# Performance work log

Hardware: AMD Instinct MI355X
Metric: run time of the kernel (lower is better)

Reference implementation:

```python
import jax, jax.numpy as jnp
import numpy as np

B, T, IN, H, L = 256, 80, 39, 256, 5


def _xavier(key, shape):
    fan_out, fan_in = shape[0], shape[1]
    std = (2.0 / (fan_in + fan_out)) ** 0.5
    return std * jax.random.normal(key, shape, dtype=jnp.float32)


def setup_inputs() -> dict:
    key = jax.random.key(0)
    ks = jax.random.split(key, 4 + 2 * L)
    x = jax.random.normal(ks[0], (B, T, IN), dtype=jnp.float32)
    # PyTorch LSTM params, gate order (i, f, g, o); biases zero per init.
    W_ih0 = _xavier(ks[1], (4 * H, IN))                       # layer 0 input weights
    W_ih_rest = jnp.stack([_xavier(ks[2 + l], (4 * H, H)) for l in range(L - 1)])  # [L-1,4H,H]
    W_hh = jnp.stack([_xavier(ks[1 + L + l], (4 * H, H)) for l in range(L)])       # [L,4H,H]
    b_ih = jnp.zeros((L, 4 * H), dtype=jnp.float32)
    b_hh = jnp.zeros((L, 4 * H), dtype=jnp.float32)
    fc_w = _xavier(ks[2 * L + 1], (1, H))
    fc_b = jnp.zeros((1,), dtype=jnp.float32)
    return {"x": x, "W_ih0": W_ih0, "W_ih_rest": W_ih_rest, "W_hh": W_hh,
            "b_ih": b_ih, "b_hh": b_hh, "fc_w": fc_w, "fc_b": fc_b}


def _lstm_layer(xs, W_ih, W_hh_l, b_ih_l, b_hh_l):
    # xs: [B,T,D]. Precompute input projection for all timesteps (one big GEMM).
    x_proj = jnp.einsum('btd,gd->btg', xs, W_ih) + b_ih_l + b_hh_l  # [B,T,4H]

    def step(carry, xp):
        h, c = carry
        gates = xp + h @ W_hh_l.T                 # [B,4H]
        i, f, g, o = jnp.split(gates, 4, axis=-1)
        c = jax.nn.sigmoid(f) * c + jax.nn.sigmoid(i) * jnp.tanh(g)
        h = jax.nn.sigmoid(o) * jnp.tanh(c)
        return (h, c), h

    b = xs.shape[0]
    h0 = jnp.zeros((b, H), dtype=xs.dtype)
    _, hs = jax.lax.scan(step, (h0, h0), jnp.swapaxes(x_proj, 0, 1))
    return jnp.swapaxes(hs, 0, 1)  # [B,T,H]


def reference(x, W_ih0, W_ih_rest, W_hh, b_ih, b_hh, fc_w, fc_b):
    h = _lstm_layer(x, W_ih0, W_hh[0], b_ih[0], b_hh[0])
    for l in range(1, L):
        h = _lstm_layer(h, W_ih_rest[l - 1], W_hh[l], b_ih[l], b_hh[l])
    out = jnp.einsum('bth,oh->bto', h, fc_w) + fc_b  # [B,T,1]
    return out[..., 0]  # [B,T]
```

## Files before the change

### kernel.cpp

```cpp
#include <hip/hip_runtime.h>

#define B_ 256
#define T_ 80
#define IN_ 39
#define H_ 256
#define G_ 1024
#define L_ 5
#define TC_ 16
#define NCH_ 5

#define XP_FLOATS   (B_ * TC_ * G_)
#define HBUF_FLOATS (B_ * T_ * H_)
#define CBUF_FLOATS (B_ * H_)
#define WG_FLOATS   (L_ * G_ * H_)
#define HX_FLOATS   (2 * 32 * 2048)
#define FLG_OFF_FLOATS (XP_FLOATS + HBUF_FLOATS + CBUF_FLOATS + WG_FLOATS + HX_FLOATS)

#define AG __HIP_MEMORY_SCOPE_AGENT
#define WG __HIP_MEMORY_SCOPE_WORKGROUP

__device__ __forceinline__ float sigm(float x) { return 1.0f / (1.0f + expf(-x)); }
__device__ __forceinline__ void fma4(float4& a, float s, const float4& w) {
    a.x = fmaf(s, w.x, a.x); a.y = fmaf(s, w.y, a.y);
    a.z = fmaf(s, w.z, a.z); a.w = fmaf(s, w.w, a.w);
}
__device__ __forceinline__ void red4(float4& a) {
    a.x += __shfl_xor(a.x, 32); a.y += __shfl_xor(a.y, 32);
    a.z += __shfl_xor(a.z, 32); a.w += __shfl_xor(a.w, 32);
}

__device__ __forceinline__ float4 ld_mall_16B(const float* p) {
    float4 v;
    asm volatile("global_load_dwordx4 %0, %1, off sc0 sc1\n\t"
                 "s_waitcnt vmcnt(0)"
                 : "=&v"(v) : "v"(p) : "memory");
    return v;
}

__device__ __forceinline__ void cbar(int* cnt, int& seq) {
    seq += 4;
    asm volatile("s_waitcnt lgkmcnt(0)" ::: "memory");
    if ((threadIdx.x & 63) == 0)
        __hip_atomic_fetch_add(cnt, 1, __ATOMIC_RELAXED, WG);
    while (__hip_atomic_load(cnt, __ATOMIC_RELAXED, WG) < seq)
        __builtin_amdgcn_s_sleep(1);
    asm volatile("s_waitcnt lgkmcnt(0)" ::: "memory");
}

extern "C" __global__ void __launch_bounds__(256)
wt_kernel(const float* __restrict__ Whh, float* __restrict__ Wg) {
    const int gid = blockIdx.x * 256 + threadIdx.x;
    const int g4 = gid & 3;
    const int j  = (gid >> 2) & 31;
    const int k  = (gid >> 7) & 255;
    const int s  = (gid >> 15) & 7;
    const int l  = gid >> 18;
    Wg[gid] = Whh[((size_t)(l * 1024 + g4 * 256 + s * 32 + j)) * 256 + k];
}

extern "C" __global__ void __launch_bounds__(256)
proj_kernel(const float* __restrict__ src, const float* __restrict__ Wih,
            const float* __restrict__ bihl, const float* __restrict__ bhhl,
            float* __restrict__ xp, int K, int t0) {
    __shared__ float As[16 * 132];
    __shared__ float Bs[16 * 68];
    const int tid = threadIdx.x;
    const int mt = blockIdx.x >> 4, nt = blockIdx.x & 15;
    const int tx = tid & 15, ty = tid >> 4;
    const int lrA = tid >> 1, lc8 = (tid & 1) * 8;
    const int lrB = tid >> 2, lc4 = (tid & 3) * 4;

    const int ar = mt * 128 + lrA;
    const int ab = ar >> 4;
    const int at = t0 + (ar & 15);
    const float* arow = src + ((size_t)ab * T_ + at) * K;
    const int brow_idx = (lrB & 3) * 256 + nt * 16 + (lrB >> 2);
    const float* brow = Wih + (size_t)brow_idx * K;

    float acc[8][4];
    #pragma unroll
    for (int i = 0; i < 8; ++i)
        #pragma unroll
        for (int j = 0; j < 4; ++j) acc[i][j] = 0.0f;

    for (int k0 = 0; k0 < K; k0 += 16) {
        __syncthreads();
        if (K == IN_) {
            #pragma unroll
            for (int i = 0; i < 8; ++i) {
                const int k = k0 + lc8 + i;
                As[(lc8 + i) * 132 + lrA] = (k < IN_) ? arow[k] : 0.0f;
            }
            #pragma unroll
            for (int i = 0; i < 4; ++i) {
                const int k = k0 + lc4 + i;
                Bs[(lc4 + i) * 68 + lrB] = (k < IN_) ? brow[k] : 0.0f;
            }
        } else {
            float4 a0 = *(const float4*)(arow + k0 + lc8);
            float4 a1 = *(const float4*)(arow + k0 + lc8 + 4);
            As[(lc8 + 0) * 132 + lrA] = a0.x;
            As[(lc8 + 1) * 132 + lrA] = a0.y;
            As[(lc8 + 2) * 132 + lrA] = a0.z;
            As[(lc8 + 3) * 132 + lrA] = a0.w;
            As[(lc8 + 4) * 132 + lrA] = a1.x;
            As[(lc8 + 5) * 132 + lrA] = a1.y;
            As[(lc8 + 6) * 132 + lrA] = a1.z;
            As[(lc8 + 7) * 132 + lrA] = a1.w;
            float4 bv = *(const float4*)(brow + k0 + lc4);
            Bs[(lc4 + 0) * 68 + lrB] = bv.x;
            Bs[(lc4 + 1) * 68 + lrB] = bv.y;
            Bs[(lc4 + 2) * 68 + lrB] = bv.z;
            Bs[(lc4 + 3) * 68 + lrB] = bv.w;
        }
        __syncthreads();
        #pragma unroll
        for (int kk = 0; kk < 16; ++kk) {
            const float4 aA = *(const float4*)&As[kk * 132 + ty * 8];
            const float4 aB = *(const float4*)&As[kk * 132 + ty * 8 + 4];
            const float4 b4 = *(const float4*)&Bs[kk * 68 + tx * 4];
            acc[0][0] += aA.x * b4.x; acc[0][1] += aA.x * b4.y;
            acc[0][2] += aA.x * b4.z; acc[0][3] += aA.x * b4.w;
            acc[1][0] += aA.y * b4.x; acc[1][1] += aA.y * b4.y;
            acc[1][2] += aA.y * b4.z; acc[1][3] += aA.y * b4.w;
            acc[2][0] += aA.z * b4.x; acc[2][1] += aA.z * b4.y;
            acc[2][2] += aA.z * b4.z; acc[2][3] += aA.z * b4.w;
            acc[3][0] += aA.w * b4.x; acc[3][1] += aA.w * b4.y;
            acc[3][2] += aA.w * b4.z; acc[3][3] += aA.w * b4.w;
            acc[4][0] += aB.x * b4.x; acc[4][1] += aB.x * b4.y;
            acc[4][2] += aB.x * b4.z; acc[4][3] += aB.x * b4.w;
            acc[5][0] += aB.y * b4.x; acc[5][1] += aB.y * b4.y;
            acc[5][2] += aB.y * b4.z; acc[5][3] += aB.y * b4.w;
            acc[6][0] += aB.z * b4.x; acc[6][1] += aB.z * b4.y;
            acc[6][2] += aB.z * b4.z; acc[6][3] += aB.z * b4.w;
            acc[7][0] += aB.w * b4.x; acc[7][1] += aB.w * b4.y;
            acc[7][2] += aB.w * b4.z; acc[7][3] += aB.w * b4.w;
        }
    }
    const int unit = nt * 16 + tx;
    const float bs0 = bihl[0 * 256 + unit] + bhhl[0 * 256 + unit];
    const float bs1 = bihl[1 * 256 + unit] + bhhl[1 * 256 + unit];
    const float bs2 = bihl[2 * 256 + unit] + bhhl[2 * 256 + unit];
    const float bs3 = bihl[3 * 256 + unit] + bhhl[3 * 256 + unit];
    #pragma unroll
    for (int i = 0; i < 8; ++i) {
        const int row = mt * 128 + ty * 8 + i;
        float4 o;
        o.x = acc[i][0] + bs0; o.y = acc[i][1] + bs1;
        o.z = acc[i][2] + bs2; o.w = acc[i][3] + bs3;
        *(float4*)&xp[(size_t)row * G_ + unit * 4] = o;
    }
}

extern "C" __global__ void __launch_bounds__(512, 2)
rec10_kernel(const float* __restrict__ xp, const float* __restrict__ Wg_l,
             float* __restrict__ hbuf, float* __restrict__ cbuf,
             float* __restrict__ hx, int* __restrict__ flg,
             int t0, int chkb, int first) {
    __shared__ float sH[2048];
    __shared__ float sP[2 * 4 * 32 * 20];
    __shared__ int   barC[2];

    const int tid = threadIdx.x;
    const int bid = blockIdx.x;
    const int grp = bid & 31;
    const int s   = bid >> 5;
    const int c   = tid >> 8;
    const int tp  = tid & 255;
    const int jj  = tp & 31;
    const int ks  = tp >> 5;
    const int w4  = tp >> 6;
    const int fb2 = tp >> 5;
    const int unit = s * 32 + jj;
    const int bglob = grp * 8 + c * 4 + (fb2 & 3);
    float* sPc = sP + c * 2560;
    int* mycnt = barC + c;
    int* flgc  = flg + (grp * 2 + c) * 32;

    if (tid < 2) barC[tid] = 0;

    const float4* Wg4 = (const float4*)Wg_l + (size_t)s * 8192;
    float4 wreg[32];
    #pragma unroll
    for (int kk = 0; kk < 32; ++kk)
        wreg[kk] = Wg4[(size_t)(ks * 32 + kk) * 32 + jj];

    float creg = 0.0f;
    if (tp < 128 && !first) creg = cbuf[(size_t)bglob * H_ + unit];

    __syncthreads();

    const float4* sH4 = (const float4*)sH;
    int seq = 0;

    for (int tt = 0; tt < TC_; ++tt) {
        const int t = t0 + tt;

        float4 xv = make_float4(0.f, 0.f, 0.f, 0.f);
        if (tp < 128)
            xv = *(const float4*)&xp[((size_t)bglob * TC_ + tt) * G_ + unit * 4];

        if (tt == 0) {
            if (first) {
                *(float4*)&sH[tp * 8 + c * 4] = make_float4(0.f, 0.f, 0.f, 0.f);
            } else {
                #pragma unroll
                for (int bb = 0; bb < 4; ++bb)
                    sH[tp * 8 + c * 4 + bb] =
                        hbuf[((size_t)(grp * 8 + c * 4 + bb) * T_ + (t0 - 1)) * H_ + tp];
            }
        } else {
            if ((tid & 63) < 8) {
                int* fp = flgc + (tid & 63);
                const int tgt = chkb + tt;
                while (__hip_atomic_load(fp, __ATOMIC_RELAXED, AG) < tgt)
                    __builtin_amdgcn_s_sleep(1);
            }
            const float* hsf = hx + (size_t)(((tt - 1) & 1) * 32 + grp) * 2048
                                  + (size_t)tp * 8 + c * 4;
            *(float4*)&sH[tp * 8 + c * 4] = ld_mall_16B(hsf);
        }
        cbar(mycnt, seq);

        float4 a0 = {0,0,0,0}, a1 = {0,0,0,0}, a2 = {0,0,0,0}, a3 = {0,0,0,0};
        #pragma unroll
        for (int kk = 0; kk < 32; ++kk) {
            const int k = ks * 32 + kk;
            const float4 wv = wreg[kk];
            const float4 hc = sH4[k * 2 + c];
            fma4(a0, hc.x, wv); fma4(a1, hc.y, wv);
            fma4(a2, hc.z, wv); fma4(a3, hc.w, wv);
        }
        red4(a0); red4(a1); red4(a2); red4(a3);
        if ((tid & 63) < 32) {
            float4* pp = (float4*)&sPc[(w4 * 32 + jj) * 20];
            pp[0] = a0; pp[1] = a1; pp[2] = a2; pp[3] = a3;
        }
        cbar(mycnt, seq);

        if (tp < 128) {
            float4 g4 = xv;
            #pragma unroll
            for (int w2 = 0; w2 < 4; ++w2) {
                const float4 pw = *(const float4*)&sPc[(w2 * 32 + jj) * 20 + fb2 * 4];
                g4.x += pw.x; g4.y += pw.y; g4.z += pw.z; g4.w += pw.w;
            }
            const float I = sigm(g4.x);
            const float F = sigm(g4.y);
            const float Gt = tanhf(g4.z);
            const float O = sigm(g4.w);
            creg = F * creg + I * Gt;
            const float hval = O * tanhf(creg);
            hbuf[((size_t)bglob * T_ + t) * H_ + unit] = hval;

            if (tt < TC_ - 1) {
                const float hpart = __shfl_xor(hval, 32);
                if ((fb2 & 1) == 0) {
                    const unsigned long long pv =
                        ((unsigned long long)__float_as_uint(hpart) << 32)
                        | __float_as_uint(hval);
                    unsigned long long* dst = (unsigned long long*)
                        (hx + (size_t)((tt & 1) * 32 + grp) * 2048
                            + unit * 8 + c * 4 + fb2);
                    __hip_atomic_store(dst, pv, __ATOMIC_RELAXED, AG);
                }
            }
        }

        if (tt < TC_ - 1) {
            asm volatile("s_waitcnt vmcnt(0)" ::: "memory");
            cbar(mycnt, seq);
            if (tp == 0)
                __hip_atomic_store(flgc + s, chkb + tt + 1, __ATOMIC_RELAXED, AG);
        }
    }

    if (tp < 128) cbuf[(size_t)bglob * H_ + unit] = creg;
}

extern "C" __global__ void __launch_bounds__(128)
fc_kernel(const float* __restrict__ hbuf, const float* __restrict__ fcw,
          const float* __restrict__ fcb, float* __restrict__ out) {
    __shared__ float wsm[256];
    const int tid = threadIdx.x;
    const int b = blockIdx.x;
    if (tid < 64) ((float4*)wsm)[tid] = ((const float4*)fcw)[tid];
    __syncthreads();
    if (tid < T_) {
        const float4* h4p = (const float4*)(hbuf + ((size_t)b * T_ + tid) * H_);
        const float4* w4p = (const float4*)wsm;
        float acc = fcb[0];
        #pragma unroll 8
        for (int k4 = 0; k4 < 64; ++k4) {
            float4 h4 = h4p[k4], w4 = w4p[k4];
            acc += h4.x * w4.x + h4.y * w4.y + h4.z * w4.z + h4.w * w4.w;
        }
        out[b * T_ + tid] = acc;
    }
}

extern "C" void kernel_launch(void* const* d_in, const int* in_sizes, int n_in,
                              void* d_out, int out_size, void* d_ws, size_t ws_size,
                              hipStream_t stream) {
    (void)in_sizes; (void)n_in; (void)out_size; (void)ws_size;
    const float* x    = (const float*)d_in[0];
    const float* Wih0 = (const float*)d_in[1];
    const float* Wihr = (const float*)d_in[2];
    const float* Whh  = (const float*)d_in[3];
    const float* bih  = (const float*)d_in[4];
    const float* bhh  = (const float*)d_in[5];
    const float* fcw  = (const float*)d_in[6];
    const float* fcb  = (const float*)d_in[7];
    float* out = (float*)d_out;
    float* ws  = (float*)d_ws;

    float* xp   = ws;
    float* hbuf = ws + XP_FLOATS;
    float* cbuf = hbuf + HBUF_FLOATS;
    float* wg   = cbuf + CBUF_FLOATS;
    float* hx   = wg + WG_FLOATS;
    int*   flg  = (int*)(ws + FLG_OFF_FLOATS);

    hipMemsetAsync(flg, 0, 64 * 32 * sizeof(int), stream);
    hipLaunchKernelGGL(wt_kernel, dim3(WG_FLOATS / 256), dim3(256), 0, stream, Whh, wg);

    for (int l = 0; l < L_; ++l) {
        const int K = (l == 0) ? IN_ : H_;
        const float* src = (l == 0) ? x : hbuf;
        const float* Wih = (l == 0) ? Wih0 : (Wihr + (size_t)(l - 1) * G_ * H_);
        const float* Wg_l = wg + (size_t)l * (G_ * H_);
        for (int ch = 0; ch < NCH_; ++ch) {
            const int t0 = ch * TC_;
            const int chkb = (l * NCH_ + ch) * (TC_ - 1);
            hipLaunchKernelGGL(proj_kernel, dim3(512), dim3(256), 0, stream,
                               src, Wih, bih + l * G_, bhh + l * G_, xp, K, t0);
            hipLaunchKernelGGL(rec10_kernel, dim3(256), dim3(512), 0, stream,
                               xp, Wg_l, hbuf, cbuf, hx, flg, t0, chkb, ch == 0 ? 1 : 0);
        }
    }
    hipLaunchKernelGGL(fc_kernel, dim3(B_), dim3(128), 0, stream, hbuf, fcw, fcb, out);
}
```

Baseline: 2.473 ms.

## Wavefront-schedule LSTM layers and chunks diagonally to run multiple layers concurrently

Replaces the sequential layer-by-chunk loop with a diagonal wavefront: each launch processes every (layer, chunk) pair on the same anti-diagonal. Each layer gets its own xp, cbuf, hx and flag buffers, so up to five layers' recurrences run in one grid. The goal is to fill more CUs (256 blocks per layer) and cut the number of serial launches from 25 pairs to 9. The chunk-boundary h is now passed through the hx exchange buffer instead of being reread from hbuf, and the block index mapping changes from grp-major to s-major. It relies on all blocks of a multi-layer grid being co-resident for the spin-wait flags, and it falls back to the old order when the workspace is too small.

```diff
diff --git a/kernel.cpp b/kernel.cpp
--- a/kernel.cpp
+++ b/kernel.cpp
@@ -14,10 +14,10 @@
 #define CBUF_FLOATS (B_ * H_)
 #define WG_FLOATS   (L_ * G_ * H_)
 #define HX_FLOATS   (2 * 32 * 2048)
-#define FLG_OFF_FLOATS (XP_FLOATS + HBUF_FLOATS + CBUF_FLOATS + WG_FLOATS + HX_FLOATS)
+#define FLG_INTS_L  2048
 
 #define AG __HIP_MEMORY_SCOPE_AGENT
-#define WG __HIP_MEMORY_SCOPE_WORKGROUP
+#define WGS __HIP_MEMORY_SCOPE_WORKGROUP
 
 __device__ __forceinline__ float sigm(float x) { return 1.0f / (1.0f + expf(-x)); }
 __device__ __forceinline__ void fma4(float4& a, float s, const float4& w) {
@@ -41,8 +41,8 @@
     seq += 4;
     asm volatile("s_waitcnt lgkmcnt(0)" ::: "memory");
     if ((threadIdx.x & 63) == 0)
-        __hip_atomic_fetch_add(cnt, 1, __ATOMIC_RELAXED, WG);
-    while (__hip_atomic_load(cnt, __ATOMIC_RELAXED, WG) < seq)
+        __hip_atomic_fetch_add(cnt, 1, __ATOMIC_RELAXED, WGS);
+    while (__hip_atomic_load(cnt, __ATOMIC_RELAXED, WGS) < seq)
         __builtin_amdgcn_s_sleep(1);
     asm volatile("s_waitcnt lgkmcnt(0)" ::: "memory");
 }
@@ -59,13 +59,28 @@
 }
 
 extern "C" __global__ void __launch_bounds__(256)
-proj_kernel(const float* __restrict__ src, const float* __restrict__ Wih,
-            const float* __restrict__ bihl, const float* __restrict__ bhhl,
-            float* __restrict__ xp, int K, int t0) {
+proj_multi(const float* __restrict__ x, const float* __restrict__ Wih0,
+           const float* __restrict__ Wihr,
+           const float* __restrict__ bih, const float* __restrict__ bhh,
+           const float* __restrict__ hbuf,
+           float* __restrict__ xp_base, unsigned long long xp_s,
+           int d, int lmin) {
     __shared__ float As[16 * 132];
     __shared__ float Bs[16 * 68];
+    const int task = blockIdx.x >> 9;
+    const int l = lmin + task;
+    const int ch = d - l;
+    const int t0 = ch * TC_;
+    const int K = (l == 0) ? IN_ : H_;
+    const float* src = (l == 0) ? x : hbuf;
+    const float* Wih = (l == 0) ? Wih0 : (Wihr + (size_t)(l - 1) * G_ * H_);
+    const float* bihl = bih + l * G_;
+    const float* bhhl = bhh + l * G_;
+    float* xp = xp_base + (size_t)l * xp_s;
+
+    const int bid9 = blockIdx.x & 511;
     const int tid = threadIdx.x;
-    const int mt = blockIdx.x >> 4, nt = blockIdx.x & 15;
+    const int mt = bid9 >> 4, nt = bid9 & 15;
     const int tx = tid & 15, ty = tid >> 4;
     const int lrA = tid >> 1, lc8 = (tid & 1) * 8;
     const int lrB = tid >> 2, lc4 = (tid & 3) * 4;
@@ -153,29 +168,44 @@
 }
 
 extern "C" __global__ void __launch_bounds__(512, 2)
-rec10_kernel(const float* __restrict__ xp, const float* __restrict__ Wg_l,
-             float* __restrict__ hbuf, float* __restrict__ cbuf,
-             float* __restrict__ hx, int* __restrict__ flg,
-             int t0, int chkb, int first) {
+rec_multi(const float* __restrict__ xp_base, unsigned long long xp_s,
+          const float* __restrict__ wg, float* __restrict__ hbuf,
+          float* __restrict__ cbuf_base, unsigned long long cb_s,
+          float* __restrict__ hx_base, unsigned long long hx_s,
+          int* __restrict__ flg_base, unsigned long long flg_s,
+          int d, int lmin) {
     __shared__ float sH[2048];
     __shared__ float sP[2 * 4 * 32 * 20];
     __shared__ int   barC[2];
 
     const int tid = threadIdx.x;
-    const int bid = blockIdx.x;
-    const int grp = bid & 31;
-    const int s   = bid >> 5;
-    const int c   = tid >> 8;
-    const int tp  = tid & 255;
-    const int jj  = tp & 31;
-    const int ks  = tp >> 5;
-    const int w4  = tp >> 6;
+    const int task = blockIdx.x >> 8;
+    const int l = lmin + task;
+    const int ch = d - l;
+    const int b8 = blockIdx.x & 255;
+    const int grp = b8 >> 3;
+    const int s   = b8 & 7;
+    const int t0 = ch * TC_;
+    const int chkb = (l * NCH_ + ch) * TC_;
+    const int first = (ch == 0);
+
+    const float* xp = xp_base + (size_t)l * xp_s;
+    const float* Wg_l = wg + (size_t)l * (G_ * H_);
+    float* cbuf = cbuf_base + (size_t)l * cb_s;
+    float* hx = hx_base + (size_t)l * hx_s;
+    int* flg = flg_base + (size_t)l * flg_s;
+
+    const int c = tid >> 8;
+    const int tp = tid & 255;
+    const int jj = tp & 31;
+    const int ks = tp >> 5;
+    const int w4 = tp >> 6;
     const int fb2 = tp >> 5;
     const int unit = s * 32 + jj;
     const int bglob = grp * 8 + c * 4 + (fb2 & 3);
     float* sPc = sP + c * 2560;
     int* mycnt = barC + c;
-    int* flgc  = flg + (grp * 2 + c) * 32;
+    int* flgc = flg + (grp * 2 + c) * 32;
 
     if (tid < 2) barC[tid] = 0;
 
@@ -200,15 +230,8 @@
         if (tp < 128)
             xv = *(const float4*)&xp[((size_t)bglob * TC_ + tt) * G_ + unit * 4];
 
-        if (tt == 0) {
-            if (first) {
-                *(float4*)&sH[tp * 8 + c * 4] = make_float4(0.f, 0.f, 0.f, 0.f);
-            } else {
-                #pragma unroll
-                for (int bb = 0; bb < 4; ++bb)
-                    sH[tp * 8 + c * 4 + bb] =
-                        hbuf[((size_t)(grp * 8 + c * 4 + bb) * T_ + (t0 - 1)) * H_ + tp];
-            }
+        if (tt == 0 && first) {
+            *(float4*)&sH[tp * 8 + c * 4] = make_float4(0.f, 0.f, 0.f, 0.f);
         } else {
             if ((tid & 63) < 8) {
                 int* fp = flgc + (tid & 63);
@@ -216,7 +239,7 @@
                 while (__hip_atomic_load(fp, __ATOMIC_RELAXED, AG) < tgt)
                     __builtin_amdgcn_s_sleep(1);
             }
-            const float* hsf = hx + (size_t)(((tt - 1) & 1) * 32 + grp) * 2048
+            const float* hsf = hx + (size_t)((((tt + 1) & 1)) * 32 + grp) * 2048
                                   + (size_t)tp * 8 + c * 4;
             *(float4*)&sH[tp * 8 + c * 4] = ld_mall_16B(hsf);
         }
@@ -253,26 +276,22 @@
             const float hval = O * tanhf(creg);
             hbuf[((size_t)bglob * T_ + t) * H_ + unit] = hval;
 
-            if (tt < TC_ - 1) {
-                const float hpart = __shfl_xor(hval, 32);
-                if ((fb2 & 1) == 0) {
-                    const unsigned long long pv =
-                        ((unsigned long long)__float_as_uint(hpart) << 32)
-                        | __float_as_uint(hval);
-                    unsigned long long* dst = (unsigned long long*)
-                        (hx + (size_t)((tt & 1) * 32 + grp) * 2048
-                            + unit * 8 + c * 4 + fb2);
-                    __hip_atomic_store(dst, pv, __ATOMIC_RELAXED, AG);
-                }
-            }
-        }
-
-        if (tt < TC_ - 1) {
-            asm volatile("s_waitcnt vmcnt(0)" ::: "memory");
-            cbar(mycnt, seq);
-            if (tp == 0)
-                __hip_atomic_store(flgc + s, chkb + tt + 1, __ATOMIC_RELAXED, AG);
-        }
+            const float hpart = __shfl_xor(hval, 32);
+            if ((fb2 & 1) == 0) {
+                const unsigned long long pv =
+                    ((unsigned long long)__float_as_uint(hpart) << 32)
+                    | __float_as_uint(hval);
+                unsigned long long* dst = (unsigned long long*)
+                    (hx + (size_t)((tt & 1) * 32 + grp) * 2048
+                        + unit * 8 + c * 4 + fb2);
+                __hip_atomic_store(dst, pv, __ATOMIC_RELAXED, AG);
+            }
+        }
+
+        asm volatile("s_waitcnt vmcnt(0)" ::: "memory");
+        cbar(mycnt, seq);
+        if (tp == 0)
+            __hip_atomic_store(flgc + s, chkb + tt + 1, __ATOMIC_RELAXED, AG);
     }
 
     if (tp < 128) cbuf[(size_t)bglob * H_ + unit] = creg;
@@ -302,7 +321,7 @@
 extern "C" void kernel_launch(void* const* d_in, const int* in_sizes, int n_in,
                               void* d_out, int out_size, void* d_ws, size_t ws_size,
                               hipStream_t stream) {
-    (void)in_sizes; (void)n_in; (void)out_size; (void)ws_size;
+    (void)in_sizes; (void)n_in; (void)out_size;
     const float* x    = (const float*)d_in[0];
     const float* Wih0 = (const float*)d_in[1];
     const float* Wihr = (const float*)d_in[2];
@@ -314,28 +333,48 @@
     float* out = (float*)d_out;
     float* ws  = (float*)d_ws;
 
+    const size_t WF_ELEMS = (size_t)5 * XP_FLOATS + HBUF_FLOATS
+                          + (size_t)5 * CBUF_FLOATS + WG_FLOATS
+                          + (size_t)5 * HX_FLOATS + (size_t)5 * FLG_INTS_L;
+    const int wf = (ws_size >= WF_ELEMS * 4) ? 1 : 0;
+
+    const unsigned long long xp_s  = wf ? XP_FLOATS   : 0;
+    const unsigned long long cb_s  = wf ? CBUF_FLOATS : 0;
+    const unsigned long long hx_s  = wf ? HX_FLOATS   : 0;
+    const unsigned long long flg_s = wf ? FLG_INTS_L  : 0;
+    const int nrep = wf ? 5 : 1;
+
     float* xp   = ws;
-    float* hbuf = ws + XP_FLOATS;
+    float* hbuf = xp + (size_t)nrep * XP_FLOATS;
     float* cbuf = hbuf + HBUF_FLOATS;
-    float* wg   = cbuf + CBUF_FLOATS;
+    float* wg   = cbuf + (size_t)nrep * CBUF_FLOATS;
     float* hx   = wg + WG_FLOATS;
-    int*   flg  = (int*)(ws + FLG_OFF_FLOATS);
-
-    hipMemsetAsync(flg, 0, 64 * 32 * sizeof(int), stream);
+    int*   flg  = (int*)(hx + (size_t)nrep * HX_FLOATS);
+
+    hipMemsetAsync(flg, 0, (size_t)nrep * FLG_INTS_L * sizeof(int), stream);
     hipLaunchKernelGGL(wt_kernel, dim3(WG_FLOATS / 256), dim3(256), 0, stream, Whh, wg);
 
-    for (int l = 0; l < L_; ++l) {
-        const int K = (l == 0) ? IN_ : H_;
-        const float* src = (l == 0) ? x : hbuf;
-        const float* Wih = (l == 0) ? Wih0 : (Wihr + (size_t)(l - 1) * G_ * H_);
-        const float* Wg_l = wg + (size_t)l * (G_ * H_);
-        for (int ch = 0; ch < NCH_; ++ch) {
-            const int t0 = ch * TC_;
-            const int chkb = (l * NCH_ + ch) * (TC_ - 1);
-            hipLaunchKernelGGL(proj_kernel, dim3(512), dim3(256), 0, stream,
-                               src, Wih, bih + l * G_, bhh + l * G_, xp, K, t0);
-            hipLaunchKernelGGL(rec10_kernel, dim3(256), dim3(512), 0, stream,
-                               xp, Wg_l, hbuf, cbuf, hx, flg, t0, chkb, ch == 0 ? 1 : 0);
+    if (wf) {
+        for (int dd = 0; dd <= L_ + NCH_ - 2; ++dd) {
+            const int lmin = (dd - (NCH_ - 1) > 0) ? (dd - (NCH_ - 1)) : 0;
+            const int lmax = (dd < L_ - 1) ? dd : (L_ - 1);
+            const int n = lmax - lmin + 1;
+            hipLaunchKernelGGL(proj_multi, dim3(n * 512), dim3(256), 0, stream,
+                               x, Wih0, Wihr, bih, bhh, hbuf, xp, xp_s, dd, lmin);
+            hipLaunchKernelGGL(rec_multi, dim3(n * 256), dim3(512), 0, stream,
+                               xp, xp_s, wg, hbuf, cbuf, cb_s, hx, hx_s,
+                               flg, flg_s, dd, lmin);
+        }
+    } else {
+        for (int l = 0; l < L_; ++l) {
+            for (int ch = 0; ch < NCH_; ++ch) {
+                const int dd = l + ch;
+                hipLaunchKernelGGL(proj_multi, dim3(512), dim3(256), 0, stream,
+                                   x, Wih0, Wihr, bih, bhh, hbuf, xp, xp_s, dd, l);
+                hipLaunchKernelGGL(rec_multi, dim3(256), dim3(512), 0, stream,
+                                   xp, xp_s, wg, hbuf, cbuf, cb_s, hx, hx_s,
+                                   flg, flg_s, dd, l);
+            }
         }
     }
     hipLaunchKernelGGL(fc_kernel, dim3(B_), dim3(128), 0, stream, hbuf, fcw, fcb, out);
```

New measurement: 2.172 ms, median of 2. 1.14x faster.
